# Performance work log

Hardware: AMD Instinct MI355X
Metric: run time of the kernel (lower is better)

The kernel has to match this reference:

```python
import jax, jax.numpy as jnp
import numpy as np

B, S, D = 1, 2048, 2048
NH, NKV = 32, 8
HD = D // NH  # 64
ROPE_THETA = 10000.0


def setup_inputs() -> dict:
    key = jax.random.key(0)
    k1, k2, k3 = jax.random.split(key, 3)
    x = jax.random.normal(k1, (B, S, D), dtype=jnp.float32)
    # real RoPE frequencies (freqs_cis = exp(i * t * theta^(-2j/hd)))
    inv_freq = 1.0 / (ROPE_THETA ** (np.arange(0, HD, 2, dtype=np.float32) / HD))
    t = np.arange(S, dtype=np.float32)
    ang = np.outer(t, inv_freq)  # [S, HD/2]
    cos = jnp.asarray(np.cos(ang), dtype=jnp.float32)
    sin = jnp.asarray(np.sin(ang), dtype=jnp.float32)
    wqkv = jax.random.normal(k2, (NH * HD + 2 * NKV * HD, D), dtype=jnp.float32) * (D ** -0.5)
    wo = jax.random.normal(k3, (D, NH * HD), dtype=jnp.float32) * (D ** -0.5)
    return {"x": x, "cos": cos, "sin": sin, "wqkv": wqkv, "wo": wo}


def _rope(t, cos, sin):
    # t: [b, h, s, hd]; pairs are interleaved (even=real, odd=imag)
    tr = t[..., 0::2]
    ti = t[..., 1::2]
    c = cos[None, None]  # [1,1,s,hd/2]
    s_ = sin[None, None]
    orr = tr * c - ti * s_
    oi = tr * s_ + ti * c
    out = jnp.stack([orr, oi], axis=-1)  # [b,h,s,hd/2,2]
    return out.reshape(t.shape)


def reference(x, cos, sin, wqkv, wo):
    bsz, seqlen, d_model = x.shape
    qkv = jnp.einsum('bsd,ed->bse', x, wqkv)  # fused QKV proj
    q, k, v = jnp.split(qkv, [NH * HD, NH * HD + NKV * HD], axis=-1)
    q = q.reshape(bsz, seqlen, NH, HD).transpose(0, 2, 1, 3)
    k = k.reshape(bsz, seqlen, NKV, HD).transpose(0, 2, 1, 3)
    v = v.reshape(bsz, seqlen, NKV, HD).transpose(0, 2, 1, 3)
    q = _rope(q, cos, sin)
    k = _rope(k, cos, sin)
    # GQA: repeat_interleave kv heads
    rep = NH // NKV
    k_r = jnp.broadcast_to(k[:, :, None], (bsz, NKV, rep, seqlen, HD)).reshape(bsz, NH, seqlen, HD)
    v_r = jnp.broadcast_to(v[:, :, None], (bsz, NKV, rep, seqlen, HD)).reshape(bsz, NH, seqlen, HD)
    scale = 1.0 / jnp.sqrt(jnp.asarray(HD, dtype=x.dtype))
    scores = jnp.einsum('bhqd,bhkd->bhqk', q, k_r) * scale
    causal = jnp.tril(jnp.ones((seqlen, seqlen), dtype=bool))
    scores = jnp.where(causal[None, None], scores, jnp.asarray(-jnp.inf, dtype=scores.dtype))
    attn = jax.nn.softmax(scores, axis=-1)
    y = jnp.einsum('bhqk,bhkd->bhqd', attn, v_r)
    y = y.transpose(0, 2, 1, 3).reshape(bsz, seqlen, NH * HD)
    y = jnp.einsum('bse,de->bsd', y, wo)
    return y
```

## Files before the change

### kernel.cpp

```cpp
#include <hip/hip_runtime.h>
#include <hip/hip_bf16.h>

typedef __attribute__((ext_vector_type(8))) short bf16x8;
typedef __attribute__((ext_vector_type(4))) float f32x4;
typedef __attribute__((ext_vector_type(16))) float f32x16;
typedef __attribute__((ext_vector_type(2))) unsigned int u32x2;

#define S_LEN 2048
#define DMODEL 2048
#define NHEAD 32
#define NKVH 8
#define HDIM 64
#define EQKV 3072

#if defined(__has_builtin)
#if __has_builtin(__builtin_amdgcn_global_load_lds)
#define HAVE_GLL 1
#endif
#endif

__device__ __forceinline__ unsigned short f2bf(float f) {
  unsigned int u = __float_as_uint(f);
  u = (u + 0x7FFFu + ((u >> 16) & 1u)) >> 16;
  return (unsigned short)u;
}

__device__ __forceinline__ f32x4 mfma16(bf16x8 a, bf16x8 b, f32x4 c) {
  return __builtin_amdgcn_mfma_f32_16x16x32_bf16(a, b, c, 0, 0, 0);
}
__device__ __forceinline__ f32x16 mfma32(bf16x8 a, bf16x8 b, f32x16 c) {
  return __builtin_amdgcn_mfma_f32_32x32x16_bf16(a, b, c, 0, 0, 0);
}

__device__ __forceinline__ unsigned cvtpk(float a, float b) {
  unsigned r;
  asm("v_cvt_pk_bf16_f32 %0, %1, %2" : "=v"(r) : "v"(a), "v"(b));
  return r;
}

__device__ __forceinline__ void plswap(unsigned& a, unsigned& b) {
  u32x2 r = __builtin_amdgcn_permlane32_swap(a, b, false, false);
  a = r.x;
  b = r.y;
}
__device__ __forceinline__ void plswapf(float& a, float& b) {
  unsigned ua = __float_as_uint(a), ub = __float_as_uint(b);
  plswap(ua, ub);
  a = __uint_as_float(ua);
  b = __uint_as_float(ub);
}

#if HAVE_GLL
__device__ __forceinline__ void gload16(const unsigned short* g,
                                        unsigned short* l) {
  __builtin_amdgcn_global_load_lds(
      (const __attribute__((address_space(1))) unsigned int*)g,
      (__attribute__((address_space(3))) unsigned int*)l, 16, 0, 0);
}
#endif

__global__ void cast_kernel(const float* __restrict__ src,
                            unsigned short* __restrict__ dst, int n4) {
  int i = blockIdx.x * blockDim.x + threadIdx.x;
  if (i >= n4) return;
  float4 v = ((const float4*)src)[i];
  ushort4 o;
  o.x = f2bf(v.x); o.y = f2bf(v.y); o.z = f2bf(v.z); o.w = f2bf(v.w);
  ((ushort4*)dst)[i] = o;
}

__launch_bounds__(256)
__global__ void gemm_bt(const unsigned short* __restrict__ A,
                        const unsigned short* __restrict__ B,
                        float* __restrict__ C, int M, int N, int K) {
  __shared__ unsigned short As[2][128 * 64];
  __shared__ unsigned short Bs[2][128 * 64];
  const int tid = threadIdx.x;
  const int w = tid >> 6, l = tid & 63;
  const int wr = w >> 1, wc = w & 1;
  const int nwg = gridDim.x * gridDim.y;
  const int bid0 = blockIdx.y * gridDim.x + blockIdx.x;
  const int swz = (bid0 & 7) * (nwg >> 3) + (bid0 >> 3);
  const int bm = swz / gridDim.x, bn = swz % gridDim.x;
  const int lr = l & 15, lq = l >> 4;

  f32x4 acc[4][4];
#pragma unroll
  for (int m = 0; m < 4; ++m)
#pragma unroll
    for (int n = 0; n < 4; ++n) acc[m][n] = (f32x4)0.f;

  const unsigned short* gA[4];
  const unsigned short* gB[4];
#pragma unroll
  for (int i = 0; i < 4; ++i) {
    int c = i * 256 + tid;
    int row = c >> 3;
    int sc = (c & 7) ^ (row & 7);
    gA[i] = A + (size_t)(bm * 128 + row) * K + sc * 8;
    gB[i] = B + (size_t)(bn * 128 + row) * K + sc * 8;
  }

#if HAVE_GLL
#define STAGE(bufi, k0)                                        \
  do {                                                         \
    _Pragma("unroll") for (int i = 0; i < 4; ++i) {            \
      gload16(gA[i] + (k0), &As[bufi][(i * 256 + w * 64) * 8]);\
      gload16(gB[i] + (k0), &Bs[bufi][(i * 256 + w * 64) * 8]);\
    }                                                          \
  } while (0)
#else
#define STAGE(bufi, k0)                                        \
  do {                                                         \
    _Pragma("unroll") for (int i = 0; i < 4; ++i) {            \
      int c = i * 256 + tid;                                   \
      *(uint4*)(&As[bufi][c * 8]) = *(const uint4*)(gA[i] + (k0)); \
      *(uint4*)(&Bs[bufi][c * 8]) = *(const uint4*)(gB[i] + (k0)); \
    }                                                          \
  } while (0)
#endif

#define COMPUTE(bufi)                                                     \
  do {                                                                    \
    _Pragma("unroll") for (int ks = 0; ks < 2; ++ks) {                    \
      bf16x8 af[4], bfr[4];                                               \
      _Pragma("unroll") for (int m = 0; m < 4; ++m) {                     \
        int row = wr * 64 + m * 16 + lr;                                  \
        int ch = (ks * 4 + lq) ^ (row & 7);                               \
        af[m] = *(const bf16x8*)(&As[bufi][row * 64 + ch * 8]);           \
      }                                                                   \
      _Pragma("unroll") for (int n = 0; n < 4; ++n) {                     \
        int row = wc * 64 + n * 16 + lr;                                  \
        int ch = (ks * 4 + lq) ^ (row & 7);                               \
        bfr[n] = *(const bf16x8*)(&Bs[bufi][row * 64 + ch * 8]);          \
      }                                                                   \
      _Pragma("unroll") for (int m = 0; m < 4; ++m)                       \
          _Pragma("unroll") for (int n = 0; n < 4; ++n)                   \
              acc[m][n] = mfma16(af[m], bfr[n], acc[m][n]);               \
    }                                                                     \
  } while (0)

  const int nt = K >> 6;
  STAGE(0, 0);
  int cur = 0;
#if HAVE_GLL
  for (int t = 0; t < nt - 1; ++t) {
    STAGE(cur ^ 1, (t + 1) * 64);
    asm volatile("s_waitcnt vmcnt(8)" ::: "memory");
    __builtin_amdgcn_sched_barrier(0);
    __builtin_amdgcn_s_barrier();
    COMPUTE(cur);
    asm volatile("s_waitcnt lgkmcnt(0)" ::: "memory");
    __builtin_amdgcn_sched_barrier(0);
    __builtin_amdgcn_s_barrier();
    cur ^= 1;
  }
  asm volatile("s_waitcnt vmcnt(0)" ::: "memory");
  __builtin_amdgcn_sched_barrier(0);
  __builtin_amdgcn_s_barrier();
  COMPUTE(cur);
#else
  for (int t = 0; t < nt; ++t) {
    if (t > 0) STAGE(cur, t * 64);
    __syncthreads();
    COMPUTE(cur);
    __syncthreads();
  }
#endif
#undef STAGE
#undef COMPUTE

  const int r0 = bm * 128 + wr * 64;
  const int c0 = bn * 128 + wc * 64;
#pragma unroll
  for (int m = 0; m < 4; ++m)
#pragma unroll
    for (int n = 0; n < 4; ++n)
#pragma unroll
      for (int r = 0; r < 4; ++r)
        C[(size_t)(r0 + m * 16 + 4 * lq + r) * N + c0 + n * 16 + lr] =
            acc[m][n][r];
}

#define KSCALE 0.18033688011112042f
__global__ void rope_split(const float* __restrict__ qkv,
                           const float* __restrict__ cosb,
                           const float* __restrict__ sinb,
                           unsigned short* __restrict__ qb,
                           unsigned short* __restrict__ kft) {
  const int s = blockIdx.x;
  const float* row = qkv + (size_t)s * EQKV;
  for (int idx = threadIdx.x; idx < 1280; idx += 256) {
    int hh = idx >> 5;
    int m = idx & 31;
    float c = cosb[s * 32 + m];
    float sn = sinb[s * 32 + m];
    if (hh < 32) {
      float tr = row[hh * 64 + 2 * m];
      float ti = row[hh * 64 + 2 * m + 1];
      unsigned int pack = (unsigned int)f2bf(tr * c - ti * sn) |
                          ((unsigned int)f2bf(tr * sn + ti * c) << 16);
      *(unsigned int*)(qb + ((size_t)hh * S_LEN + s) * HDIM + 2 * m) = pack;
    } else {
      int kvh = hh - 32;
      float cs = c * KSCALE, ss = sn * KSCALE;
      float tr = row[2048 + kvh * 64 + 2 * m];
      float ti = row[2048 + kvh * 64 + 2 * m + 1];
      unsigned int pack = (unsigned int)f2bf(tr * cs - ti * ss) |
                          ((unsigned int)f2bf(tr * ss + ti * cs) << 16);
      int kt = s >> 5, lq = s & 31;
      int j = m >> 3, hi = (m >> 2) & 1;
      unsigned short* dst =
          kft +
          ((((size_t)kvh * 64 + kt) * 4 + j) * 64 + lq + 32 * hi) * 8 +
          (m & 3) * 2;
      *(unsigned int*)dst = pack;
    }
  }
}

__global__ void v_transpose(const float* __restrict__ qkv,
                            unsigned short* __restrict__ vft) {
  __shared__ unsigned short tile[64][72];
  const int kvh = blockIdx.x;
  const int st = blockIdx.y;
  const int t = threadIdx.x;
  {
    const int sl = t >> 2, dg = t & 3;
    const float* src =
        qkv + (size_t)(st * 64 + sl) * EQKV + 2560 + kvh * 64 + dg * 16;
#pragma unroll
    for (int j = 0; j < 16; ++j) tile[dg * 16 + j][sl] = f2bf(src[j]);
  }
  __syncthreads();
  {
    const int kt_local = t >> 7, c = (t >> 5) & 3, lq2 = t & 31;
    const int kt = st * 2 + kt_local;
    const int d = ((c >> 1) & 1) * 32 + lq2;
    unsigned short* dbase =
        vft + (((size_t)(kvh * 64 + kt) * 4 + c) * 64) * 8;
#pragma unroll
    for (int hi2 = 0; hi2 < 2; ++hi2) {
      int koff = kt_local * 32 + (c & 1) * 16 + 8 * hi2;
      *(uint4*)(dbase + (lq2 + 32 * hi2) * 8) =
          *(const uint4*)(&tile[d][koff]);
    }
  }
}

__launch_bounds__(256, 4)
__global__ void attn_kernel(const unsigned short* __restrict__ qb,
                            const unsigned short* __restrict__ kft,
                            const unsigned short* __restrict__ vft,
                            unsigned short* __restrict__ aob) {
  __shared__ float buf[4][64][19];
  const int tid = threadIdx.x;
  const int wv = tid >> 6, l = tid & 63;
  const int bid = blockIdx.x;
  const int h = bid & 31;
  const int qt = 63 - (bid >> 5);
  const int kvh = h >> 2;
  const int q0 = qt << 5;
  const int lq = l & 31;
  const int hi = l >> 5;
  const int qg = q0 + lq;

  const unsigned short* qrow = qb + ((size_t)h * S_LEN + qg) * HDIM + 8 * hi;
  bf16x8 qf[4];
#pragma unroll
  for (int j = 0; j < 4; ++j) qf[j] = *(const bf16x8*)(qrow + 16 * j);

  const unsigned short* kbase = kft + (size_t)kvh * 64 * 2048;
  const unsigned short* vbase = vft + (size_t)kvh * 64 * 2048;

  f32x16 o0 = (f32x16)0.f, o1 = (f32x16)0.f;
  float mrun = -1e30f, lrun = 0.f;
  const int ntile = qt + 1;

  for (int kt = wv; kt < ntile; kt += 4) {
    const int key0 = kt << 5;
    const unsigned short* kvt = kbase + (size_t)kt * 2048;
    bf16x8 kf0 = *(const bf16x8*)(kvt + l * 8);
    bf16x8 kf1 = *(const bf16x8*)(kvt + 512 + l * 8);
    bf16x8 kf2 = *(const bf16x8*)(kvt + 1024 + l * 8);
    bf16x8 kf3 = *(const bf16x8*)(kvt + 1536 + l * 8);
    const unsigned short* vvt = vbase + (size_t)kt * 2048;
    bf16x8 va00 = *(const bf16x8*)(vvt + l * 8);
    bf16x8 va01 = *(const bf16x8*)(vvt + 512 + l * 8);
    bf16x8 va10 = *(const bf16x8*)(vvt + 1024 + l * 8);
    bf16x8 va11 = *(const bf16x8*)(vvt + 1536 + l * 8);

    f32x16 s = (f32x16)0.f;
    __builtin_amdgcn_s_setprio(1);
    s = mfma32(kf0, qf[0], s);
    s = mfma32(kf1, qf[1], s);
    s = mfma32(kf2, qf[2], s);
    s = mfma32(kf3, qf[3], s);
    __builtin_amdgcn_s_setprio(0);

    float p[16];
    if (kt == ntile - 1) {
#pragma unroll
      for (int r = 0; r < 16; ++r) {
        int key = key0 + (r & 3) + 8 * (r >> 2) + 4 * hi;
        p[r] = (key > qg) ? -1e30f : s[r];
      }
    } else {
#pragma unroll
      for (int r = 0; r < 16; ++r) p[r] = s[r];
    }
    float a0 = fmaxf(fmaxf(p[0], p[1]), p[2]);
    float a1 = fmaxf(fmaxf(p[3], p[4]), p[5]);
    float a2 = fmaxf(fmaxf(p[6], p[7]), p[8]);
    float a3 = fmaxf(fmaxf(p[9], p[10]), p[11]);
    float a4 = fmaxf(fmaxf(p[12], p[13]), p[14]);
    float mt = fmaxf(fmaxf(fmaxf(a0, a1), a2), fmaxf(fmaxf(a3, a4), p[15]));
    float mto = mt;
    plswapf(mt, mto);
    mt = fmaxf(mt, mto);
    if (!__all(mt - mrun <= 8.f)) {
      float mnew = fmaxf(mrun, mt);
      float al = __builtin_amdgcn_exp2f(mrun - mnew);
      mrun = mnew;
      lrun *= al;
      o0 *= al;
      o1 *= al;
    }
#pragma unroll
    for (int r = 0; r < 16; ++r) p[r] = __builtin_amdgcn_exp2f(p[r] - mrun);
    float s0 = (p[0] + p[1]) + (p[2] + p[3]);
    float s1 = (p[4] + p[5]) + (p[6] + p[7]);
    float s2 = (p[8] + p[9]) + (p[10] + p[11]);
    float s3 = (p[12] + p[13]) + (p[14] + p[15]);
    float ts = (s0 + s1) + (s2 + s3);
    float tso = ts;
    plswapf(ts, tso);
    ts += tso;
    lrun += ts;
    union B8 { unsigned u[4]; bf16x8 v; } pb0, pb1;
    {
      unsigned t0 = cvtpk(p[0], p[1]), t1 = cvtpk(p[4], p[5]);
      plswap(t0, t1);
      pb0.u[0] = t0; pb0.u[2] = t1;
    }
    {
      unsigned t0 = cvtpk(p[2], p[3]), t1 = cvtpk(p[6], p[7]);
      plswap(t0, t1);
      pb0.u[1] = t0; pb0.u[3] = t1;
    }
    {
      unsigned t0 = cvtpk(p[8], p[9]), t1 = cvtpk(p[12], p[13]);
      plswap(t0, t1);
      pb1.u[0] = t0; pb1.u[2] = t1;
    }
    {
      unsigned t0 = cvtpk(p[10], p[11]), t1 = cvtpk(p[14], p[15]);
      plswap(t0, t1);
      pb1.u[1] = t0; pb1.u[3] = t1;
    }
    __builtin_amdgcn_s_setprio(1);
    o0 = mfma32(va00, pb0.v, o0);
    o0 = mfma32(va01, pb1.v, o0);
    o1 = mfma32(va10, pb0.v, o1);
    o1 = mfma32(va11, pb1.v, o1);
    __builtin_amdgcn_s_setprio(0);
  }

  {
    union F16 { f32x16 v; f32x4 q[4]; } uu;
    uu.v = o0;
    float* dst = &buf[wv][l][0];
#pragma unroll
    for (int i = 0; i < 4; ++i) *(f32x4*)(dst + 4 * i) = uu.q[i];
    dst[16] = mrun;
    dst[17] = lrun;
  }
  __syncthreads();
  float mfin = -1e30f;
#pragma unroll
  for (int w2 = 0; w2 < 4; ++w2) mfin = fmaxf(mfin, buf[w2][l][16]);
  float lsum = 0.f;
  float scl[4];
#pragma unroll
  for (int w2 = 0; w2 < 4; ++w2) {
    scl[w2] = __builtin_amdgcn_exp2f(buf[w2][l][16] - mfin);
    lsum += buf[w2][l][17] * scl[w2];
  }
  const float inv = 1.f / lsum;
  unsigned short* obase = aob + (size_t)qg * DMODEL + h * 64;
  {
    f32x4 acc = (f32x4)0.f;
#pragma unroll
    for (int w2 = 0; w2 < 4; ++w2)
      acc += *(const f32x4*)&buf[w2][l][wv * 4] * scl[w2];
    unsigned u0 = cvtpk(acc[0] * inv, acc[1] * inv);
    unsigned u1 = cvtpk(acc[2] * inv, acc[3] * inv);
    unsigned short* dsto = obase + 8 * wv + 4 * hi;
    *(unsigned*)(dsto) = u0;
    *(unsigned*)(dsto + 2) = u1;
  }
  __syncthreads();
  {
    union F16 { f32x16 v; f32x4 q[4]; } uu;
    uu.v = o1;
    float* dst = &buf[wv][l][0];
#pragma unroll
    for (int i = 0; i < 4; ++i) *(f32x4*)(dst + 4 * i) = uu.q[i];
  }
  __syncthreads();
  {
    f32x4 acc = (f32x4)0.f;
#pragma unroll
    for (int w2 = 0; w2 < 4; ++w2)
      acc += *(const f32x4*)&buf[w2][l][wv * 4] * scl[w2];
    unsigned u0 = cvtpk(acc[0] * inv, acc[1] * inv);
    unsigned u1 = cvtpk(acc[2] * inv, acc[3] * inv);
    unsigned short* dsto = obase + 32 + 8 * wv + 4 * hi;
    *(unsigned*)(dsto) = u0;
    *(unsigned*)(dsto + 2) = u1;
  }
}

extern "C" void kernel_launch(void* const* d_in, const int* in_sizes, int n_in,
                              void* d_out, int out_size, void* d_ws,
                              size_t ws_size, hipStream_t stream) {
  const float* x = (const float*)d_in[0];
  const float* cosb = (const float*)d_in[1];
  const float* sinb = (const float*)d_in[2];
  const float* wqkv = (const float*)d_in[3];
  const float* wo = (const float*)d_in[4];
  float* out = (float*)d_out;
  char* ws = (char*)d_ws;
  float* qkv = (float*)(ws);
  unsigned short* xb = (unsigned short*)(ws + 25165824);
  unsigned short* wb = (unsigned short*)(ws + 33554432);
  unsigned short* wob = (unsigned short*)(ws + 46137344);
  unsigned short* qb = (unsigned short*)(ws + 54525952);
  unsigned short* kft = (unsigned short*)(ws + 62914560);
  unsigned short* vft = (unsigned short*)(ws + 65011712);
  unsigned short* aob = (unsigned short*)(ws + 67108864);

  cast_kernel<<<dim3(1048576 / 256), 256, 0, stream>>>(x, xb, 1048576);
  cast_kernel<<<dim3(1572864 / 256), 256, 0, stream>>>(wqkv, wb, 1572864);
  cast_kernel<<<dim3(1048576 / 256), 256, 0, stream>>>(wo, wob, 1048576);
  gemm_bt<<<dim3(24, 16), 256, 0, stream>>>(xb, wb, qkv, 2048, 3072, 2048);
  rope_split<<<dim3(2048), 256, 0, stream>>>(qkv, cosb, sinb, qb, kft);
  v_transpose<<<dim3(8, 32), 256, 0, stream>>>(qkv, vft);
  attn_kernel<<<dim3(2048), 256, 0, stream>>>(qb, kft, vft, aob);
  gemm_bt<<<dim3(16, 16), 256, 0, stream>>>(aob, wob, out, 2048, 2048, 2048);
}
```

Measured before the change: 134.5 us.

## Fuse cast launches, shrink GEMM N-tile, unroll attention key loop by two

The three fp32-to-bf16 casts now run in one launch, removing two launches. The GEMM tile drops from 128x128 to 128x64, which doubles the grid so more workgroups fill the CUs, at the cost of more A-tile reloads from memory. The attention kernel handles two key tiles per iteration, loading both sets of K and V up front to expose more memory-level parallelism and to amortize the softmax max and rescale work. Its occupancy hint drops from 4 to 3 waves to make room for the extra registers.

Result: faster. 121.6 us (-9.6%).

```diff
diff --git a/kernel.cpp b/kernel.cpp
--- a/kernel.cpp
+++ b/kernel.cpp
@@ -59,14 +59,27 @@
 }
 #endif
 
-__global__ void cast_kernel(const float* __restrict__ src,
-                            unsigned short* __restrict__ dst, int n4) {
+__global__ void cast3_kernel(const float* __restrict__ x,
+                             const float* __restrict__ wqkv,
+                             const float* __restrict__ wo,
+                             unsigned short* __restrict__ xb,
+                             unsigned short* __restrict__ wb,
+                             unsigned short* __restrict__ wob) {
   int i = blockIdx.x * blockDim.x + threadIdx.x;
-  if (i >= n4) return;
-  float4 v = ((const float4*)src)[i];
+  const float* s;
+  unsigned short* d;
+  int j;
+  if (i < 1048576) {
+    s = x; d = xb; j = i;
+  } else if (i < 2621440) {
+    s = wqkv; d = wb; j = i - 1048576;
+  } else {
+    s = wo; d = wob; j = i - 2621440;
+  }
+  float4 v = ((const float4*)s)[j];
   ushort4 o;
   o.x = f2bf(v.x); o.y = f2bf(v.y); o.z = f2bf(v.z); o.w = f2bf(v.w);
-  ((ushort4*)dst)[i] = o;
+  ((ushort4*)d)[j] = o;
 }
 
 __launch_bounds__(256)
@@ -74,7 +87,7 @@
                         const unsigned short* __restrict__ B,
                         float* __restrict__ C, int M, int N, int K) {
   __shared__ unsigned short As[2][128 * 64];
-  __shared__ unsigned short Bs[2][128 * 64];
+  __shared__ unsigned short Bs[2][64 * 64];
   const int tid = threadIdx.x;
   const int w = tid >> 6, l = tid & 63;
   const int wr = w >> 1, wc = w & 1;
@@ -84,58 +97,67 @@
   const int bm = swz / gridDim.x, bn = swz % gridDim.x;
   const int lr = l & 15, lq = l >> 4;
 
-  f32x4 acc[4][4];
+  f32x4 acc[4][2];
 #pragma unroll
   for (int m = 0; m < 4; ++m)
 #pragma unroll
-    for (int n = 0; n < 4; ++n) acc[m][n] = (f32x4)0.f;
+    for (int n = 0; n < 2; ++n) acc[m][n] = (f32x4)0.f;
 
   const unsigned short* gA[4];
-  const unsigned short* gB[4];
+  const unsigned short* gB[2];
 #pragma unroll
   for (int i = 0; i < 4; ++i) {
     int c = i * 256 + tid;
     int row = c >> 3;
     int sc = (c & 7) ^ (row & 7);
     gA[i] = A + (size_t)(bm * 128 + row) * K + sc * 8;
-    gB[i] = B + (size_t)(bn * 128 + row) * K + sc * 8;
+  }
+#pragma unroll
+  for (int i = 0; i < 2; ++i) {
+    int c = i * 256 + tid;
+    int row = c >> 3;
+    int sc = (c & 7) ^ (row & 7);
+    gB[i] = B + (size_t)(bn * 64 + row) * K + sc * 8;
   }
 
 #if HAVE_GLL
-#define STAGE(bufi, k0)                                        \
-  do {                                                         \
-    _Pragma("unroll") for (int i = 0; i < 4; ++i) {            \
-      gload16(gA[i] + (k0), &As[bufi][(i * 256 + w * 64) * 8]);\
-      gload16(gB[i] + (k0), &Bs[bufi][(i * 256 + w * 64) * 8]);\
-    }                                                          \
+#define STAGE(bufi, k0)                                            \
+  do {                                                             \
+    _Pragma("unroll") for (int i = 0; i < 4; ++i)                  \
+        gload16(gA[i] + (k0), &As[bufi][(i * 256 + w * 64) * 8]);  \
+    _Pragma("unroll") for (int i = 0; i < 2; ++i)                  \
+        gload16(gB[i] + (k0), &Bs[bufi][(i * 256 + w * 64) * 8]);  \
   } while (0)
 #else
-#define STAGE(bufi, k0)                                        \
-  do {                                                         \
-    _Pragma("unroll") for (int i = 0; i < 4; ++i) {            \
-      int c = i * 256 + tid;                                   \
+#define STAGE(bufi, k0)                                            \
+  do {                                                             \
+    _Pragma("unroll") for (int i = 0; i < 4; ++i) {                \
+      int c = i * 256 + tid;                                       \
       *(uint4*)(&As[bufi][c * 8]) = *(const uint4*)(gA[i] + (k0)); \
+    }                                                              \
+    _Pragma("unroll") for (int i = 0; i < 2; ++i) {                \
+      int c = i * 256 + tid;                                       \
       *(uint4*)(&Bs[bufi][c * 8]) = *(const uint4*)(gB[i] + (k0)); \
-    }                                                          \
+    }                                                              \
   } while (0)
 #endif
 
 #define COMPUTE(bufi)                                                     \
   do {                                                                    \
     _Pragma("unroll") for (int ks = 0; ks < 2; ++ks) {                    \
-      bf16x8 af[4], bfr[4];                                               \
+      bf16x8 af[4], bfr[2];                                               \
       _Pragma("unroll") for (int m = 0; m < 4; ++m) {                     \
         int row = wr * 64 + m * 16 + lr;                                  \
         int ch = (ks * 4 + lq) ^ (row & 7);                               \
         af[m] = *(const bf16x8*)(&As[bufi][row * 64 + ch * 8]);           \
       }                                                                   \
-      _Pragma("unroll") for (int n = 0; n < 4; ++n) {                     \
-        int row = wc * 64 + n * 16 + lr;                                  \
+      _Pragma("unroll") for (int n = 0; n < 2; ++n) {                     \
+        int row = wc * 32 + n * 16 + lr;                                  \
         int ch = (ks * 4 + lq) ^ (row & 7);                               \
         bfr[n] = *(const bf16x8*)(&Bs[bufi][row * 64 + ch * 8]);          \
       }                                                                   \
       _Pragma("unroll") for (int m = 0; m < 4; ++m)                       \
-          _Pragma("unroll") for (int n = 0; n < 4; ++n)                   \
+          _Pragma("unroll") for (int n = 0; n < 2; ++n)                   \
               acc[m][n] = mfma16(af[m], bfr[n], acc[m][n]);               \
     }                                                                     \
   } while (0)
@@ -146,7 +168,7 @@
 #if HAVE_GLL
   for (int t = 0; t < nt - 1; ++t) {
     STAGE(cur ^ 1, (t + 1) * 64);
-    asm volatile("s_waitcnt vmcnt(8)" ::: "memory");
+    asm volatile("s_waitcnt vmcnt(6)" ::: "memory");
     __builtin_amdgcn_sched_barrier(0);
     __builtin_amdgcn_s_barrier();
     COMPUTE(cur);
@@ -171,11 +193,11 @@
 #undef COMPUTE
 
   const int r0 = bm * 128 + wr * 64;
-  const int c0 = bn * 128 + wc * 64;
+  const int c0 = bn * 64 + wc * 32;
 #pragma unroll
   for (int m = 0; m < 4; ++m)
 #pragma unroll
-    for (int n = 0; n < 4; ++n)
+    for (int n = 0; n < 2; ++n)
 #pragma unroll
       for (int r = 0; r < 4; ++r)
         C[(size_t)(r0 + m * 16 + 4 * lq + r) * N + c0 + n * 16 + lr] =
@@ -248,7 +270,7 @@
   }
 }
 
-__launch_bounds__(256, 4)
+__launch_bounds__(256, 3)
 __global__ void attn_kernel(const unsigned short* __restrict__ qb,
                             const unsigned short* __restrict__ kft,
                             const unsigned short* __restrict__ vft,
@@ -277,7 +299,132 @@
   float mrun = -1e30f, lrun = 0.f;
   const int ntile = qt + 1;
 
-  for (int kt = wv; kt < ntile; kt += 4) {
+  int kt = wv;
+  for (; kt + 4 < ntile; kt += 8) {
+    const unsigned short* ka = kbase + (size_t)kt * 2048;
+    const unsigned short* va = vbase + (size_t)kt * 2048;
+    bf16x8 kfa[4], kfb[4], vaa[4], vab[4];
+#pragma unroll
+    for (int j = 0; j < 4; ++j) {
+      kfa[j] = *(const bf16x8*)(ka + 512 * j + l * 8);
+      kfb[j] = *(const bf16x8*)(ka + 4 * 2048 + 512 * j + l * 8);
+      vaa[j] = *(const bf16x8*)(va + 512 * j + l * 8);
+      vab[j] = *(const bf16x8*)(va + 4 * 2048 + 512 * j + l * 8);
+    }
+    f32x16 sa = (f32x16)0.f, sb = (f32x16)0.f;
+    __builtin_amdgcn_s_setprio(1);
+#pragma unroll
+    for (int j = 0; j < 4; ++j) sa = mfma32(kfa[j], qf[j], sa);
+#pragma unroll
+    for (int j = 0; j < 4; ++j) sb = mfma32(kfb[j], qf[j], sb);
+    __builtin_amdgcn_s_setprio(0);
+
+    float p[32];
+#pragma unroll
+    for (int r = 0; r < 16; ++r) p[r] = sa[r];
+    if (kt + 4 == ntile - 1) {
+#pragma unroll
+      for (int r = 0; r < 16; ++r) {
+        int key = (kt + 4) * 32 + (r & 3) + 8 * (r >> 2) + 4 * hi;
+        p[16 + r] = (key > qg) ? -1e30f : sb[r];
+      }
+    } else {
+#pragma unroll
+      for (int r = 0; r < 16; ++r) p[16 + r] = sb[r];
+    }
+    float a0 = fmaxf(fmaxf(p[0], p[1]), p[2]);
+    float a1 = fmaxf(fmaxf(p[3], p[4]), p[5]);
+    float a2 = fmaxf(fmaxf(p[6], p[7]), p[8]);
+    float a3 = fmaxf(fmaxf(p[9], p[10]), p[11]);
+    float a4 = fmaxf(fmaxf(p[12], p[13]), p[14]);
+    float b0 = fmaxf(fmaxf(p[15], p[16]), p[17]);
+    float b1 = fmaxf(fmaxf(p[18], p[19]), p[20]);
+    float b2 = fmaxf(fmaxf(p[21], p[22]), p[23]);
+    float b3 = fmaxf(fmaxf(p[24], p[25]), p[26]);
+    float b4 = fmaxf(fmaxf(p[27], p[28]), p[29]);
+    float b5 = fmaxf(p[30], p[31]);
+    float mt = fmaxf(fmaxf(fmaxf(fmaxf(a0, a1), fmaxf(a2, a3)),
+                           fmaxf(fmaxf(a4, b0), fmaxf(b1, b2))),
+                     fmaxf(fmaxf(b3, b4), b5));
+    float mto = mt;
+    plswapf(mt, mto);
+    mt = fmaxf(mt, mto);
+    if (!__all(mt - mrun <= 8.f)) {
+      float mnew = fmaxf(mrun, mt);
+      float al = __builtin_amdgcn_exp2f(mrun - mnew);
+      mrun = mnew;
+      lrun *= al;
+      o0 *= al;
+      o1 *= al;
+    }
+#pragma unroll
+    for (int r = 0; r < 32; ++r) p[r] = __builtin_amdgcn_exp2f(p[r] - mrun);
+    float s0 = (p[0] + p[1]) + (p[2] + p[3]);
+    float s1 = (p[4] + p[5]) + (p[6] + p[7]);
+    float s2 = (p[8] + p[9]) + (p[10] + p[11]);
+    float s3 = (p[12] + p[13]) + (p[14] + p[15]);
+    float s4 = (p[16] + p[17]) + (p[18] + p[19]);
+    float s5 = (p[20] + p[21]) + (p[22] + p[23]);
+    float s6 = (p[24] + p[25]) + (p[26] + p[27]);
+    float s7 = (p[28] + p[29]) + (p[30] + p[31]);
+    float ts = ((s0 + s1) + (s2 + s3)) + ((s4 + s5) + (s6 + s7));
+    float tso = ts;
+    plswapf(ts, tso);
+    ts += tso;
+    lrun += ts;
+    union B8 { unsigned u[4]; bf16x8 v; } pb0a, pb1a, pb0b, pb1b;
+    {
+      unsigned t0 = cvtpk(p[0], p[1]), t1 = cvtpk(p[4], p[5]);
+      plswap(t0, t1);
+      pb0a.u[0] = t0; pb0a.u[2] = t1;
+    }
+    {
+      unsigned t0 = cvtpk(p[2], p[3]), t1 = cvtpk(p[6], p[7]);
+      plswap(t0, t1);
+      pb0a.u[1] = t0; pb0a.u[3] = t1;
+    }
+    {
+      unsigned t0 = cvtpk(p[8], p[9]), t1 = cvtpk(p[12], p[13]);
+      plswap(t0, t1);
+      pb1a.u[0] = t0; pb1a.u[2] = t1;
+    }
+    {
+      unsigned t0 = cvtpk(p[10], p[11]), t1 = cvtpk(p[14], p[15]);
+      plswap(t0, t1);
+      pb1a.u[1] = t0; pb1a.u[3] = t1;
+    }
+    {
+      unsigned t0 = cvtpk(p[16], p[17]), t1 = cvtpk(p[20], p[21]);
+      plswap(t0, t1);
+      pb0b.u[0] = t0; pb0b.u[2] = t1;
+    }
+    {
+      unsigned t0 = cvtpk(p[18], p[19]), t1 = cvtpk(p[22], p[23]);
+      plswap(t0, t1);
+      pb0b.u[1] = t0; pb0b.u[3] = t1;
+    }
+    {
+      unsigned t0 = cvtpk(p[24], p[25]), t1 = cvtpk(p[28], p[29]);
+      plswap(t0, t1);
+      pb1b.u[0] = t0; pb1b.u[2] = t1;
+    }
+    {
+      unsigned t0 = cvtpk(p[26], p[27]), t1 = cvtpk(p[30], p[31]);
+      plswap(t0, t1);
+      pb1b.u[1] = t0; pb1b.u[3] = t1;
+    }
+    __builtin_amdgcn_s_setprio(1);
+    o0 = mfma32(vaa[0], pb0a.v, o0);
+    o0 = mfma32(vaa[1], pb1a.v, o0);
+    o1 = mfma32(vaa[2], pb0a.v, o1);
+    o1 = mfma32(vaa[3], pb1a.v, o1);
+    o0 = mfma32(vab[0], pb0b.v, o0);
+    o0 = mfma32(vab[1], pb1b.v, o0);
+    o1 = mfma32(vab[2], pb0b.v, o1);
+    o1 = mfma32(vab[3], pb1b.v, o1);
+    __builtin_amdgcn_s_setprio(0);
+  }
+  if (kt < ntile) {
     const int key0 = kt << 5;
     const unsigned short* kvt = kbase + (size_t)kt * 2048;
     bf16x8 kf0 = *(const bf16x8*)(kvt + l * 8);
@@ -440,12 +587,11 @@
   unsigned short* vft = (unsigned short*)(ws + 65011712);
   unsigned short* aob = (unsigned short*)(ws + 67108864);
 
-  cast_kernel<<<dim3(1048576 / 256), 256, 0, stream>>>(x, xb, 1048576);
-  cast_kernel<<<dim3(1572864 / 256), 256, 0, stream>>>(wqkv, wb, 1572864);
-  cast_kernel<<<dim3(1048576 / 256), 256, 0, stream>>>(wo, wob, 1048576);
-  gemm_bt<<<dim3(24, 16), 256, 0, stream>>>(xb, wb, qkv, 2048, 3072, 2048);
+  cast3_kernel<<<dim3(3670016 / 256), 256, 0, stream>>>(x, wqkv, wo, xb, wb,
+                                                        wob);
+  gemm_bt<<<dim3(48, 16), 256, 0, stream>>>(xb, wb, qkv, 2048, 3072, 2048);
   rope_split<<<dim3(2048), 256, 0, stream>>>(qkv, cosb, sinb, qb, kft);
   v_transpose<<<dim3(8, 32), 256, 0, stream>>>(qkv, vft);
   attn_kernel<<<dim3(2048), 256, 0, stream>>>(qb, kft, vft, aob);
-  gemm_bt<<<dim3(16, 16), 256, 0, stream>>>(aob, wob, out, 2048, 2048, 2048);
-}
+  gemm_bt<<<dim3(32, 16), 256, 0, stream>>>(aob, wob, out, 2048, 2048, 2048);
+}
```
